# Optimization experiments

Measured on AMD Instinct MI355X. Metric: run time of the kernel, lower is better.

The kernel has to match this reference:

```python
import jax, jax.numpy as jnp
import numpy as np

N, E, R, F, HD = 4096, 2048, 4, 128, 256
DEG_EPS = 1e-8
BN_EPS = 1e-5
LN_EPS = 1e-5


def _xavier(k, shape):
    scale = np.sqrt(2.0 / (shape[-2] + shape[-1])).astype(np.float32)
    return jax.random.normal(k, shape, jnp.float32) * scale


def setup_inputs() -> dict:
    key = jax.random.key(0)
    ks = jax.random.split(key, 8)
    X = jax.random.normal(ks[0], (N, F), jnp.float32)
    # sparse binary incidence matrices, one per relation type, stacked [R,N,E]
    H = (jax.random.uniform(ks[1], (R, N, E)) < 0.05).astype(jnp.float32)
    return {
        "X": X,
        "H": H,
        "W1": _xavier(ks[2], (R, F, HD)),
        "W2": _xavier(ks[3], (R, HD, HD)),
        "W3": _xavier(ks[4], (R, HD, F)),
        "imp": jnp.ones((3, R), jnp.float32),        # relation_importance per conv layer
        "b1": jnp.zeros((HD,), jnp.float32),
        "b2": jnp.zeros((HD,), jnp.float32),
        "b3": jnp.zeros((F,), jnp.float32),
        "bn_gamma": jnp.ones((2, HD), jnp.float32),
        "bn_beta": jnp.zeros((2, HD), jnp.float32),
        "ln_gamma": jnp.ones((2, HD), jnp.float32),
        "ln_beta": jnp.zeros((2, HD), jnp.float32),
        "rel_attn": jnp.ones((R,), jnp.float32) / R,
    }


def typed_conv(X, Hw, W, imp, bias):
    # Hw: [R,N,E] weighted incidence; theta = Dv^{-1/2} H De^{-1/2} via row/col scaling
    dv = jnp.power(Hw.sum(axis=2) + DEG_EPS, -0.5)   # [R,N]
    de = jnp.power(Hw.sum(axis=1) + DEG_EPS, -0.5)   # [R,E]
    theta = Hw * dv[:, :, None] * de[:, None, :]     # [R,N,E]
    # (theta @ theta^T) @ X computed as theta @ (theta^T @ X) -- same math, no NxN
    t = jnp.einsum('rne,nf->ref', theta, X)          # [R,E,Fin]
    Hn = jnp.einsum('rne,ref->rnf', theta, t)        # [R,N,Fin]
    out = jnp.einsum('rnf,rfo->rno', Hn, W)          # [R,N,Fout]
    out = out * jax.nn.sigmoid(imp)[:, None, None]
    return out.sum(axis=0) + bias


def bn_ln_elu(X, bg, bb, lg, lb):
    # BatchNorm1d with batch statistics (biased var), then LayerNorm, then ELU
    mu = X.mean(axis=0)
    var = X.var(axis=0)
    X = (X - mu) * jax.lax.rsqrt(var + BN_EPS) * bg + bb
    m = X.mean(axis=-1, keepdims=True)
    v = X.var(axis=-1, keepdims=True)
    X = (X - m) * jax.lax.rsqrt(v + LN_EPS) * lg + lb
    return jax.nn.elu(X)


def reference(X, H, W1, W2, W3, imp, b1, b2, b3, bn_gamma, bn_beta, ln_gamma, ln_beta, rel_attn):
    rw = jax.nn.softmax(rel_attn)
    Hw = H * rw[:, None, None]                       # weighted incidence per relation
    h = typed_conv(X, Hw, W1, imp[0], b1)
    h = bn_ln_elu(h, bn_gamma[0], bn_beta[0], ln_gamma[0], ln_beta[0])
    h = typed_conv(h, Hw, W2, imp[1], b2)
    h = bn_ln_elu(h, bn_gamma[1], bn_beta[1], ln_gamma[1], ln_beta[1])
    out = typed_conv(h, Hw, W3, imp[2], b3)
    return out + X  # residual: out_channels == in_channels by construction
```

## Files before the change

### kernel.cpp

```cpp
#include <hip/hip_runtime.h>
#include <hip/hip_bf16.h>

#define NN 4096
#define EE 2048
#define RR 4
#define FF 128
#define HDD 256
#define S1 192
#define S2 320

typedef __attribute__((ext_vector_type(4))) float floatx4;
typedef __attribute__((ext_vector_type(8))) __bf16 bf16x8;
typedef __attribute__((ext_vector_type(8))) unsigned short u16x8;

#define AS1 __attribute__((address_space(1)))
#define AS3 __attribute__((address_space(3)))

__device__ __forceinline__ void async16(const void* g, void* l) {
  __builtin_amdgcn_global_load_lds((const AS1 void*)(unsigned long long)(g),
                                   (AS3 void*)(unsigned int)(unsigned long long)(l),
                                   16, 0, 0);
}

__device__ inline unsigned short f2b(float x) {
  unsigned int u = __float_as_uint(x);
  unsigned int r = u + 0x7fffu + ((u >> 16) & 1u);
  return (unsigned short)(r >> 16);
}

__device__ inline float rel_w(const float* rel, int r) {
  float m = fmaxf(fmaxf(rel[0], rel[1]), fmaxf(rel[2], rel[3]));
  float s = 0.f;
#pragma unroll
  for (int i = 0; i < RR; i++) s += expf(rel[i] - m);
  return expf(rel[r] - m) / s;
}

__global__ void k_prep1(const float* __restrict__ H, const float* __restrict__ rel,
                        const float* __restrict__ W1, const float* __restrict__ W2,
                        const float* __restrict__ W3, const float* __restrict__ imp,
                        float* __restrict__ dvs, unsigned long long* __restrict__ mask,
                        unsigned short* __restrict__ idx1, int* __restrict__ cnt1,
                        unsigned short* __restrict__ W1catT, unsigned short* __restrict__ W2T,
                        unsigned short* __restrict__ W3T, int* __restrict__ cnt2) {
  int b = blockIdx.x;
  if (b < 4096) {
    int wave = (b << 2) | (threadIdx.x >> 6);
    int lane = threadIdx.x & 63;
    int r = wave >> 12;
    const float* row = H + (size_t)wave * EE;
    unsigned long long* mrow = mask + (size_t)wave * 32;
    unsigned short* list = idx1 + (size_t)wave * S1;
    int tot = 0;
    for (int j = 0; j < 32; j++) {
      float h = row[j * 64 + lane];
      unsigned long long m = __ballot(h != 0.0f);
      if (lane == 0) mrow[j] = m;
      if (h != 0.0f) {
        int pos = tot + __popcll(m & ((1ull << lane) - 1ull));
        if (pos < S1) list[pos] = (unsigned short)(j * 64 + lane);
      }
      tot += __popcll(m);
    }
    int tc = tot < S1 ? tot : S1;
    int padded = (tc + 7) & ~7;
    if (padded == 0) padded = 8;
    unsigned short padE = (unsigned short)((RR - r) << 11);
    if (lane < padded - tc) list[tc + lane] = padE;
    if (lane == 0) {
      cnt1[wave] = tc;
      float rwr = rel_w(rel, r);
      dvs[wave] = rwr * rsqrtf(rwr * (float)tot + 1e-8f);
    }
  } else if (b < 4096 + 2048) {
    int idx = (b - 4096) * 256 + threadIdx.x;
    if (idx < RR * FF * HDD) {
      int o = idx % HDD, f = (idx / HDD) % FF, r = idx / (HDD * FF);
      float sg = 1.0f / (1.0f + expf(-imp[r]));
      W1catT[(size_t)o * (RR * FF) + r * FF + f] = f2b(sg * W1[((size_t)r * FF + f) * HDD + o]);
    } else if (idx < RR * FF * HDD + RR * HDD * HDD) {
      int j = idx - RR * FF * HDD;
      int c = j % HDD, o = (j / HDD) % HDD, r = j / (HDD * HDD);
      float sg = 1.0f / (1.0f + expf(-imp[RR + r]));
      W2T[j] = f2b(sg * W2[((size_t)r * HDD + c) * HDD + o]);
    } else {
      int j = idx - RR * FF * HDD - RR * HDD * HDD;
      int c = j % HDD, o = (j / HDD) % FF, r = j / (HDD * FF);
      float sg = 1.0f / (1.0f + expf(-imp[2 * RR + r]));
      W3T[j] = f2b(sg * W3[((size_t)r * HDD + c) * FF + o]);
    }
  } else {
    int i = (b - 6144) * 256 + threadIdx.x;
    if (i < RR * EE) cnt2[i] = 0;
  }
}

__global__ void k_prep2(const unsigned long long* __restrict__ m1, int* __restrict__ cnt2,
                        unsigned short* __restrict__ idx2, const float* __restrict__ X,
                        const float* __restrict__ dvs, unsigned short* __restrict__ Xdv) {
  __shared__ unsigned long long w[64 * 33];
  int t = threadIdx.x;
  if (blockIdx.x < 256) {
    int r = blockIdx.x >> 6;
    int n0 = (blockIdx.x & 63) << 6;
    const unsigned long long* src = m1 + ((size_t)(r << 12) + n0) * 32;
#pragma unroll
    for (int i = 0; i < 8; i++) {
      int idx = t + i * 256;
      int n = idx >> 5, W = idx & 31;
      w[n * 33 + W] = src[idx];
    }
    __syncthreads();
    int wid = t >> 6, lane = t & 63;
#pragma unroll
    for (int Wi = 0; Wi < 8; Wi++) {
      int W = wid * 8 + Wi;
      unsigned long long myw = w[lane * 33 + W];
      unsigned long long out = 0;
      for (int bb = 0; bb < 64; bb++) {
        unsigned long long mm = __ballot(((myw >> bb) & 1ull) != 0);
        if (lane == bb) out = mm;
      }
      if (out) {
        int e = W * 64 + lane;
        int rowid = (r << 11) + e;
        int c = __popcll(out);
        int off = atomicAdd(&cnt2[rowid], c);
        unsigned long long bb2 = out;
        while (bb2) {
          int l = __builtin_ctzll(bb2);
          bb2 &= bb2 - 1;
          if (off < S2) idx2[(size_t)rowid * S2 + off] = (unsigned short)(n0 + l);
          off++;
        }
      }
    }
  } else {
    int g = (blockIdx.x - 256) * 256 + t;
    int f8 = g & 15, n = (g >> 4) & (NN - 1), r = g >> 16;
    const float* xp = X + (size_t)n * FF + (f8 << 3);
    float4 v0 = *(const float4*)xp;
    float4 v1 = *(const float4*)(xp + 4);
    float d = dvs[(r << 12) + n];
    ushort4 o0, o1;
    o0.x = f2b(v0.x * d); o0.y = f2b(v0.y * d); o0.z = f2b(v0.z * d); o0.w = f2b(v0.w * d);
    o1.x = f2b(v1.x * d); o1.y = f2b(v1.y * d); o1.z = f2b(v1.z * d); o1.w = f2b(v1.w * d);
    unsigned short* dp = Xdv + ((size_t)(r << 12) + n) * FF + (f8 << 3);
    *(ushort4*)dp = o0;
    *(ushort4*)(dp + 4) = o1;
  }
}

__global__ void k_prep3(int* __restrict__ cnt2, unsigned short* __restrict__ idx2,
                        unsigned short* __restrict__ Xdv, unsigned short* __restrict__ hwdv,
                        unsigned short* __restrict__ ydv, unsigned short* __restrict__ t1,
                        unsigned short* __restrict__ t2, unsigned short* __restrict__ t3,
                        unsigned short* __restrict__ Z1) {
  int b = blockIdx.x, t = threadIdx.x;
  if (b < 32) {
    int row = (b << 8) + t;
    int r = row >> 11;
    int cnt = cnt2[row];
    if (cnt > S2) { cnt = S2; cnt2[row] = S2; }
    int padded = (cnt + 7) & ~7;
    if (padded == 0) padded = 8;
    unsigned short pv = (unsigned short)((RR - r) << 12);
    for (int i = cnt; i < padded; i++) idx2[(size_t)row * S2 + i] = pv;
  } else {
    int q = b - 32;
    unsigned short* p; int C;
    switch (q) {
      case 0: p = Xdv  + (size_t)(RR * NN) * FF;  C = FF;  break;
      case 1: p = hwdv + (size_t)(RR * NN) * HDD; C = HDD; break;
      case 2: p = ydv  + (size_t)(RR * NN) * FF;  C = FF;  break;
      case 3: p = t1   + (size_t)(RR * EE) * FF;  C = FF;  break;
      case 4: p = t2   + (size_t)(RR * EE) * HDD; C = HDD; break;
      case 5: p = t3   + (size_t)(RR * EE) * FF;  C = FF;  break;
      default: p = Z1  + (size_t)(RR * EE) * HDD; C = HDD; break;
    }
    if (t < C) p[t] = 0;
  }
}

__global__ __launch_bounds__(256) void k_gemm3(
    const unsigned short* __restrict__ A, const unsigned short* __restrict__ BT,
    int K, int lda, int ldb, long a_rs, long b_rs,
    unsigned short* __restrict__ P, long c_rs, int ldc,
    const float* __restrict__ rscale, long rs_rs) {
  __shared__ unsigned short Al[2][128 * 64];
  __shared__ unsigned short Bl[2][128 * 64];
  int tid = threadIdx.x, wid = tid >> 6, lane = tid & 63;
  int m0 = blockIdx.x << 7, n0 = blockIdx.y << 7;
  int zr = blockIdx.z;
  int r8 = lane >> 3, c8 = lane & 7;
  int swz = ((c8 ^ r8) << 3);
  const unsigned short* Ab = A + (size_t)zr * a_rs + (size_t)m0 * lda;
  const unsigned short* Bb = BT + (size_t)zr * b_rs + (size_t)n0 * ldb;
  auto stage = [&](int pb, int k0) {
#pragma unroll
    for (int t = 0; t < 4; t++) {
      int rbase = (wid << 5) + (t << 3);
      int row = rbase + r8;
      async16(Ab + (size_t)row * lda + k0 + swz, &Al[pb][rbase * 64 + lane * 8]);
      async16(Bb + (size_t)row * ldb + k0 + swz, &Bl[pb][rbase * 64 + lane * 8]);
    }
  };
  int wm = (wid >> 1) << 6, wn = (wid & 1) << 6;
  int fm = lane & 15, quad = lane >> 4;
  int f7 = fm & 7;
  floatx4 acc[4][4];
#pragma unroll
  for (int i = 0; i < 4; i++)
#pragma unroll
    for (int j = 0; j < 4; j++) acc[i][j] = (floatx4){0.f, 0.f, 0.f, 0.f};
  auto compute = [&](int pb) {
#pragma unroll
    for (int ks = 0; ks < 2; ks++) {
      int kg = (ks << 2) | quad;
      int ko = ((kg ^ f7) << 3);
      bf16x8 a[4], b[4];
#pragma unroll
      for (int i = 0; i < 4; i++) {
        a[i] = *(const bf16x8*)&Al[pb][(wm + i * 16 + fm) * 64 + ko];
        b[i] = *(const bf16x8*)&Bl[pb][(wn + i * 16 + fm) * 64 + ko];
      }
#pragma unroll
      for (int i = 0; i < 4; i++)
#pragma unroll
        for (int j = 0; j < 4; j++)
          acc[i][j] = __builtin_amdgcn_mfma_f32_16x16x32_bf16(a[i], b[j], acc[i][j], 0, 0, 0);
    }
  };
  stage(0, 0);
  __syncthreads();
  for (int k0 = 0; k0 < K; k0 += 128) {
    if (k0 + 64 < K) stage(1, k0 + 64);
    compute(0);
    __syncthreads();
    if (k0 + 128 < K) stage(0, k0 + 128);
    compute(1);
    __syncthreads();
  }
  unsigned short* Cb = P + (size_t)zr * c_rs;
#pragma unroll
  for (int mi = 0; mi < 4; mi++)
#pragma unroll
    for (int v = 0; v < 4; v++) {
      int row = m0 + wm + mi * 16 + quad * 4 + v;
      float rs = rscale ? rscale[(size_t)zr * rs_rs + row] : 1.0f;
#pragma unroll
      for (int ni = 0; ni < 4; ni++) {
        int col = n0 + wn + ni * 16 + fm;
        Cb[(size_t)row * ldc + col] = f2b(acc[mi][ni][v] * rs);
      }
    }
}

template <int C>
__global__ __launch_bounds__(256) void k_b2s(
    const int* __restrict__ cnt2, const unsigned short* __restrict__ idx2,
    const unsigned short* __restrict__ T, const float* __restrict__ rel,
    unsigned short* __restrict__ out, float* __restrict__ csz) {
  if (blockIdx.x == 0) { csz[threadIdx.x] = 0.f; csz[threadIdx.x + 256] = 0.f; }
  int wid = threadIdx.x >> 6, lane = threadIdx.x & 63;
  int wv = (blockIdx.x << 2) | wid;
  int r = wv >> 11;
  int cnt = cnt2[wv];
  const unsigned short* list = idx2 + (size_t)wv * S2;
  const unsigned short* Tb = T + ((size_t)(r << 12)) * C;
  int lo = (C == 256) ? (lane << 2) : (lane << 1);
  float a0 = 0.f, a1 = 0.f, a2 = 0.f, a3 = 0.f;
  int nb = (cnt + 7) >> 3;
  uint2 u[8];
  {
    u16x8 I = *(const u16x8*)list;
#pragma unroll
    for (int k = 0; k < 8; k++) {
      const unsigned short* p = Tb + (size_t)((unsigned short)I[k]) * C + lo;
      if (C == 256) u[k] = *(const uint2*)p;
      else { u[k].x = *(const unsigned int*)p; u[k].y = 0; }
    }
  }
  for (int b = 0; b < nb; b++) {
    int bn = (b + 1 < nb) ? b + 1 : b;
    u16x8 I = *(const u16x8*)(list + (bn << 3));
    uint2 un[8];
#pragma unroll
    for (int k = 0; k < 8; k++) {
      const unsigned short* p = Tb + (size_t)((unsigned short)I[k]) * C + lo;
      if (C == 256) un[k] = *(const uint2*)p;
      else { un[k].x = *(const unsigned int*)p; un[k].y = 0; }
    }
#pragma unroll
    for (int k = 0; k < 8; k++) {
      a0 += __uint_as_float(u[k].x << 16);
      a1 += __uint_as_float(u[k].x & 0xffff0000u);
      if (C == 256) {
        a2 += __uint_as_float(u[k].y << 16);
        a3 += __uint_as_float(u[k].y & 0xffff0000u);
      }
    }
#pragma unroll
    for (int k = 0; k < 8; k++) u[k] = un[k];
  }
  float rwr = rel_w(rel, r);
  float s = 1.0f / (rwr * (float)cnt + 1e-8f);
  unsigned short* op = out + (size_t)wv * C;
  if (C == 256) {
    ushort4 o;
    o.x = f2b(a0 * s); o.y = f2b(a1 * s); o.z = f2b(a2 * s); o.w = f2b(a3 * s);
    *(ushort4*)(op + (lane << 2)) = o;
  } else {
    ushort2 o;
    o.x = f2b(a0 * s); o.y = f2b(a1 * s);
    *(ushort2*)(op + (lane << 1)) = o;
  }
}

__global__ __launch_bounds__(256) void k_b1s256(
    const int* __restrict__ cnt1, const unsigned short* __restrict__ idx1,
    const unsigned short* __restrict__ T, const float* __restrict__ dvs,
    float* __restrict__ out) {
  __shared__ float sm[4][256];
  int wid = threadIdx.x >> 6, lane = threadIdx.x & 63;
  int n = blockIdx.x;
  int rn = (wid << 12) + n;
  int cnt = cnt1[rn];
  const unsigned short* list = idx1 + (size_t)rn * S1;
  const unsigned short* Tb = T + ((size_t)(wid << 11)) * 256;
  float a0 = 0.f, a1 = 0.f, a2 = 0.f, a3 = 0.f;
  int nb = (cnt + 7) >> 3;
  uint2 u[8];
  {
    u16x8 I = *(const u16x8*)list;
#pragma unroll
    for (int k = 0; k < 8; k++)
      u[k] = *(const uint2*)(Tb + (size_t)((unsigned short)I[k]) * 256 + (lane << 2));
  }
  for (int b = 0; b < nb; b++) {
    int bn = (b + 1 < nb) ? b + 1 : b;
    u16x8 I = *(const u16x8*)(list + (bn << 3));
    uint2 un[8];
#pragma unroll
    for (int k = 0; k < 8; k++)
      un[k] = *(const uint2*)(Tb + (size_t)((unsigned short)I[k]) * 256 + (lane << 2));
#pragma unroll
    for (int k = 0; k < 8; k++) {
      a0 += __uint_as_float(u[k].x << 16);
      a1 += __uint_as_float(u[k].x & 0xffff0000u);
      a2 += __uint_as_float(u[k].y << 16);
      a3 += __uint_as_float(u[k].y & 0xffff0000u);
    }
#pragma unroll
    for (int k = 0; k < 8; k++) u[k] = un[k];
  }
  float dv = dvs[rn];
  float4 yv = {dv * a0, dv * a1, dv * a2, dv * a3};
  *(float4*)&sm[wid][lane << 2] = yv;
  __syncthreads();
  int c = threadIdx.x;
  out[(size_t)n * HDD + c] = sm[0][c] + sm[1][c] + sm[2][c] + sm[3][c];
}

__global__ __launch_bounds__(256) void k_b1s128o(
    const int* __restrict__ cnt1, const unsigned short* __restrict__ idx1,
    const unsigned short* __restrict__ T, const float* __restrict__ dvs,
    const float* __restrict__ X, const float* __restrict__ b3, float* __restrict__ out) {
  __shared__ float sm[4][128];
  int wid = threadIdx.x >> 6, lane = threadIdx.x & 63;
  int n = blockIdx.x;
  int rn = (wid << 12) + n;
  int cnt = cnt1[rn];
  const unsigned short* list = idx1 + (size_t)rn * S1;
  const unsigned short* Tb = T + ((size_t)(wid << 11)) * 128;
  float a0 = 0.f, a1 = 0.f;
  int nb = (cnt + 7) >> 3;
  unsigned int u[8];
  {
    u16x8 I = *(const u16x8*)list;
#pragma unroll
    for (int k = 0; k < 8; k++)
      u[k] = *(const unsigned int*)(Tb + (size_t)((unsigned short)I[k]) * 128 + (lane << 1));
  }
  for (int b = 0; b < nb; b++) {
    int bn = (b + 1 < nb) ? b + 1 : b;
    u16x8 I = *(const u16x8*)(list + (bn << 3));
    unsigned int un[8];
#pragma unroll
    for (int k = 0; k < 8; k++)
      un[k] = *(const unsigned int*)(Tb + (size_t)((unsigned short)I[k]) * 128 + (lane << 1));
#pragma unroll
    for (int k = 0; k < 8; k++) {
      a0 += __uint_as_float(u[k] << 16);
      a1 += __uint_as_float(u[k] & 0xffff0000u);
    }
#pragma unroll
    for (int k = 0; k < 8; k++) u[k] = un[k];
  }
  float dv = dvs[rn];
  float2 yv = {dv * a0, dv * a1};
  *(float2*)&sm[wid][lane << 1] = yv;
  __syncthreads();
  int t = threadIdx.x;
  if (t < 128) {
    float y = sm[0][t] + sm[1][t] + sm[2][t] + sm[3][t];
    out[(size_t)n * FF + t] = X[(size_t)n * FF + t] + b3[t] + y;
  }
}

__global__ void k_stats(const float* __restrict__ x, float* __restrict__ cs) {
  __shared__ float sm[2][8][256];
  int cg = (threadIdx.x & 31) << 3;
  int rowt = threadIdx.x >> 5;
  int r0 = blockIdx.x * 32;
  float s[8] = {0, 0, 0, 0, 0, 0, 0, 0}, s2[8] = {0, 0, 0, 0, 0, 0, 0, 0};
  for (int j = 0; j < 4; j++) {
    const float* p = x + (size_t)(r0 + rowt * 4 + j) * HDD + cg;
    float4 v0 = *(const float4*)p;
    float4 v1 = *(const float4*)(p + 4);
    float vv[8] = {v0.x, v0.y, v0.z, v0.w, v1.x, v1.y, v1.z, v1.w};
#pragma unroll
    for (int i = 0; i < 8; i++) { s[i] += vv[i]; s2[i] += vv[i] * vv[i]; }
  }
#pragma unroll
  for (int i = 0; i < 8; i++) { sm[0][rowt][cg + i] = s[i]; sm[1][rowt][cg + i] = s2[i]; }
  __syncthreads();
  int c = threadIdx.x;
  float a0 = 0, a1 = 0;
#pragma unroll
  for (int t = 0; t < 8; t++) { a0 += sm[0][t][c]; a1 += sm[1][t][c]; }
  atomicAdd(&cs[c], a0);
  atomicAdd(&cs[c + 256], a1);
}

__global__ void k_bnlnelu(const float* __restrict__ x, const float* __restrict__ cs,
                          const float* __restrict__ bg, const float* __restrict__ bb,
                          const float* __restrict__ lg, const float* __restrict__ lb,
                          unsigned short* __restrict__ out) {
  int wid = threadIdx.x >> 6, lane = threadIdx.x & 63;
  int n = blockIdx.x * 4 + wid;
  float y[4];
  float m = 0.f;
#pragma unroll
  for (int j = 0; j < 4; j++) {
    int c = lane + 64 * j;
    float mu = cs[c] * (1.0f / NN);
    float var = cs[c + 256] * (1.0f / NN) - mu * mu;
    float xv = x[(size_t)n * HDD + c];
    y[j] = (xv - mu) * rsqrtf(var + 1e-5f) * bg[c] + bb[c];
    m += y[j];
  }
  for (int off = 32; off; off >>= 1) m += __shfl_down(m, off);
  m = __shfl(m, 0) * (1.0f / HDD);
  float var = 0.f;
#pragma unroll
  for (int j = 0; j < 4; j++) { float d = y[j] - m; var += d * d; }
  for (int off = 32; off; off >>= 1) var += __shfl_down(var, off);
  var = __shfl(var, 0) * (1.0f / HDD);
  float inv = rsqrtf(var + 1e-5f);
#pragma unroll
  for (int j = 0; j < 4; j++) {
    int c = lane + 64 * j;
    float z = (y[j] - m) * inv * lg[c] + lb[c];
    z = z > 0.f ? z : expm1f(z);
    out[(size_t)n * HDD + c] = f2b(z);
  }
}

extern "C" void kernel_launch(void* const* d_in, const int* in_sizes, int n_in,
                              void* d_out, int out_size, void* d_ws, size_t ws_size,
                              hipStream_t stream) {
  const float* X   = (const float*)d_in[0];
  const float* H   = (const float*)d_in[1];
  const float* W1  = (const float*)d_in[2];
  const float* W2  = (const float*)d_in[3];
  const float* W3  = (const float*)d_in[4];
  const float* imp = (const float*)d_in[5];
  const float* b3  = (const float*)d_in[8];
  const float* bng = (const float*)d_in[9];
  const float* bnb = (const float*)d_in[10];
  const float* lng = (const float*)d_in[11];
  const float* lnb = (const float*)d_in[12];
  const float* rel = (const float*)d_in[13];
  (void)in_sizes; (void)n_in; (void)out_size; (void)ws_size;

  char* w = (char*)d_ws;
  size_t off = 0;
  auto alloc = [&](size_t bytes) -> void* {
    void* p = w + off;
    off += (bytes + 255) & ~(size_t)255;
    return p;
  };
  float* dvs   = (float*)alloc((size_t)RR * NN * 4);
  float* csbuf = (float*)alloc(512 * 4);
  int* cnt1    = (int*)alloc((size_t)RR * NN * 4);
  int* cnt2    = (int*)alloc((size_t)RR * EE * 4);
  unsigned long long* mask1 = (unsigned long long*)alloc((size_t)RR * NN * 32 * 8);
  unsigned short* idx1 = (unsigned short*)alloc((size_t)RR * NN * S1 * 2);
  unsigned short* idx2 = (unsigned short*)alloc((size_t)RR * EE * S2 * 2);
  unsigned short* Xdv  = (unsigned short*)alloc(((size_t)RR * NN + 1) * FF * 2);
  unsigned short* t1   = (unsigned short*)alloc(((size_t)RR * EE + 1) * FF * 2);
  unsigned short* Z1   = (unsigned short*)alloc(((size_t)RR * EE + 1) * HDD * 2);
  float* convout       = (float*)alloc((size_t)NN * HDD * 4);
  unsigned short* Xb   = (unsigned short*)alloc((size_t)NN * HDD * 2);
  unsigned short* hwdv = (unsigned short*)alloc(((size_t)RR * NN + 1) * HDD * 2);
  unsigned short* t2   = (unsigned short*)alloc(((size_t)RR * EE + 1) * HDD * 2);
  unsigned short* ydv  = (unsigned short*)alloc(((size_t)RR * NN + 1) * FF * 2);
  unsigned short* t3   = (unsigned short*)alloc(((size_t)RR * EE + 1) * FF * 2);
  unsigned short* W1catT = (unsigned short*)alloc((size_t)RR * FF * HDD * 2);
  unsigned short* W2T    = (unsigned short*)alloc((size_t)RR * HDD * HDD * 2);
  unsigned short* W3T    = (unsigned short*)alloc((size_t)RR * HDD * FF * 2);

  k_prep1<<<4096 + 2048 + 32, 256, 0, stream>>>(H, rel, W1, W2, W3, imp,
                                                dvs, mask1, idx1, cnt1, W1catT, W2T, W3T, cnt2);
  k_prep2<<<256 + 1024, 256, 0, stream>>>(mask1, cnt2, idx2, X, dvs, Xdv);
  k_prep3<<<32 + 7, 256, 0, stream>>>(cnt2, idx2, Xdv, hwdv, ydv, t1, t2, t3, Z1);

  k_b2s<128><<<2048, 256, 0, stream>>>(cnt2, idx2, Xdv, rel, t1, csbuf);
  k_gemm3<<<dim3(EE / 128, HDD / 128, RR), 256, 0, stream>>>(
      t1, W1catT, FF, FF, RR * FF, (long)EE * FF, FF, Z1, (long)EE * HDD, HDD, nullptr, 0);
  k_b1s256<<<NN, 256, 0, stream>>>(cnt1, idx1, Z1, dvs, convout);
  k_stats<<<NN / 32, 256, 0, stream>>>(convout, csbuf);
  k_bnlnelu<<<NN / 4, 256, 0, stream>>>(convout, csbuf, bng, bnb, lng, lnb, Xb);

  k_gemm3<<<dim3(NN / 128, HDD / 128, RR), 256, 0, stream>>>(
      Xb, W2T, HDD, HDD, HDD, 0, (long)HDD * HDD, hwdv, (long)NN * HDD, HDD, dvs, NN);
  k_b2s<256><<<2048, 256, 0, stream>>>(cnt2, idx2, hwdv, rel, t2, csbuf);
  k_b1s256<<<NN, 256, 0, stream>>>(cnt1, idx1, t2, dvs, convout);
  k_stats<<<NN / 32, 256, 0, stream>>>(convout, csbuf);
  k_bnlnelu<<<NN / 4, 256, 0, stream>>>(convout, csbuf, bng + HDD, bnb + HDD, lng + HDD, lnb + HDD, Xb);

  k_gemm3<<<dim3(NN / 128, 1, RR), 256, 0, stream>>>(
      Xb, W3T, HDD, HDD, HDD, 0, (long)FF * HDD, ydv, (long)NN * FF, FF, dvs, NN);
  k_b2s<128><<<2048, 256, 0, stream>>>(cnt2, idx2, ydv, rel, t3, csbuf);
  k_b1s128o<<<NN, 256, 0, stream>>>(cnt1, idx1, t3, dvs, X, b3, (float*)d_out);
}
```

Baseline: 565.0 us.

## Double-buffer gather loops, remap b2s blocks per XCD, fuse BN stats into gather

The sparse-gather kernels now alternate between two register buffers, so the gathers for two batches ahead are in flight while the current one accumulates. Index lists are padded to at least 24 so the pipeline prologue stays in bounds. k_b2s maps blocks so that each XCD handles one relation's half of the edges, aiming for better L2 locality. The separate column-statistics kernel is removed; k_b1s256 atomically adds column sums and sums of squares into 8 striped partial buffers, which the BN kernel then adds together. This removes one pass over convout and one launch per layer, at the cost of more atomics and more register pressure.

```diff
diff --git a/kernel.cpp b/kernel.cpp
--- a/kernel.cpp
+++ b/kernel.cpp
@@ -64,7 +64,7 @@
     }
     int tc = tot < S1 ? tot : S1;
     int padded = (tc + 7) & ~7;
-    if (padded == 0) padded = 8;
+    if (padded < 24) padded = 24;
     unsigned short padE = (unsigned short)((RR - r) << 11);
     if (lane < padded - tc) list[tc + lane] = padE;
     if (lane == 0) {
@@ -163,7 +163,7 @@
     int cnt = cnt2[row];
     if (cnt > S2) { cnt = S2; cnt2[row] = S2; }
     int padded = (cnt + 7) & ~7;
-    if (padded == 0) padded = 8;
+    if (padded < 24) padded = 24;
     unsigned short pv = (unsigned short)((RR - r) << 12);
     for (int i = cnt; i < padded; i++) idx2[(size_t)row * S2 + i] = pv;
   } else {
@@ -261,47 +261,58 @@
     const int* __restrict__ cnt2, const unsigned short* __restrict__ idx2,
     const unsigned short* __restrict__ T, const float* __restrict__ rel,
     unsigned short* __restrict__ out, float* __restrict__ csz) {
-  if (blockIdx.x == 0) { csz[threadIdx.x] = 0.f; csz[threadIdx.x + 256] = 0.f; }
+  if (blockIdx.x == 0) {
+#pragma unroll
+    for (int i = 0; i < 16; i++) csz[i * 256 + threadIdx.x] = 0.f;
+  }
   int wid = threadIdx.x >> 6, lane = threadIdx.x & 63;
-  int wv = (blockIdx.x << 2) | wid;
-  int r = wv >> 11;
+  int bid = blockIdx.x;
+  int xcd = bid & 7;
+  int r = xcd >> 1;
+  int e = ((xcd & 1) << 10) + ((bid >> 3) << 2) + wid;
+  int wv = (r << 11) + e;
   int cnt = cnt2[wv];
   const unsigned short* list = idx2 + (size_t)wv * S2;
   const unsigned short* Tb = T + ((size_t)(r << 12)) * C;
   int lo = (C == 256) ? (lane << 2) : (lane << 1);
   float a0 = 0.f, a1 = 0.f, a2 = 0.f, a3 = 0.f;
   int nb = (cnt + 7) >> 3;
-  uint2 u[8];
-  {
-    u16x8 I = *(const u16x8*)list;
+  if (nb < 3) nb = 3;
+  uint2 u[8], v[8];
+  auto LIDX = [&](int bo) { return *(const u16x8*)(list + (bo << 3)); };
+  auto GATH = [&](uint2 (&d)[8], u16x8 I) {
 #pragma unroll
     for (int k = 0; k < 8; k++) {
       const unsigned short* p = Tb + (size_t)((unsigned short)I[k]) * C + lo;
-      if (C == 256) u[k] = *(const uint2*)p;
-      else { u[k].x = *(const unsigned int*)p; u[k].y = 0; }
-    }
-  }
-  for (int b = 0; b < nb; b++) {
-    int bn = (b + 1 < nb) ? b + 1 : b;
-    u16x8 I = *(const u16x8*)(list + (bn << 3));
-    uint2 un[8];
+      if (C == 256) d[k] = *(const uint2*)p;
+      else d[k].x = *(const unsigned int*)p;
+    }
+  };
+  auto ACCU = [&](uint2 (&d)[8]) {
 #pragma unroll
     for (int k = 0; k < 8; k++) {
-      const unsigned short* p = Tb + (size_t)((unsigned short)I[k]) * C + lo;
-      if (C == 256) un[k] = *(const uint2*)p;
-      else { un[k].x = *(const unsigned int*)p; un[k].y = 0; }
-    }
-#pragma unroll
-    for (int k = 0; k < 8; k++) {
-      a0 += __uint_as_float(u[k].x << 16);
-      a1 += __uint_as_float(u[k].x & 0xffff0000u);
+      a0 += __uint_as_float(d[k].x << 16);
+      a1 += __uint_as_float(d[k].x & 0xffff0000u);
       if (C == 256) {
-        a2 += __uint_as_float(u[k].y << 16);
-        a3 += __uint_as_float(u[k].y & 0xffff0000u);
+        a2 += __uint_as_float(d[k].y << 16);
+        a3 += __uint_as_float(d[k].y & 0xffff0000u);
       }
     }
-#pragma unroll
-    for (int k = 0; k < 8; k++) u[k] = un[k];
+  };
+  u16x8 iA = LIDX(0), iB = LIDX(1);
+  GATH(u, iA);
+  iA = LIDX(2);
+  GATH(v, iB);
+  iB = LIDX(3 < nb - 1 ? 3 : nb - 1);
+  for (int b = 0; b < nb; b += 2) {
+    ACCU(u);
+    if (b + 2 < nb) GATH(u, iA);
+    if (b + 4 < nb) iA = LIDX(b + 4);
+    if (b + 1 < nb) {
+      ACCU(v);
+      if (b + 3 < nb) GATH(v, iB);
+      if (b + 5 < nb) iB = LIDX(b + 5);
+    }
   }
   float rwr = rel_w(rel, r);
   float s = 1.0f / (rwr * (float)cnt + 1e-8f);
@@ -320,7 +331,7 @@
 __global__ __launch_bounds__(256) void k_b1s256(
     const int* __restrict__ cnt1, const unsigned short* __restrict__ idx1,
     const unsigned short* __restrict__ T, const float* __restrict__ dvs,
-    float* __restrict__ out) {
+    float* __restrict__ out, float* __restrict__ csbuf) {
   __shared__ float sm[4][256];
   int wid = threadIdx.x >> 6, lane = threadIdx.x & 63;
   int n = blockIdx.x;
@@ -330,36 +341,48 @@
   const unsigned short* Tb = T + ((size_t)(wid << 11)) * 256;
   float a0 = 0.f, a1 = 0.f, a2 = 0.f, a3 = 0.f;
   int nb = (cnt + 7) >> 3;
-  uint2 u[8];
-  {
-    u16x8 I = *(const u16x8*)list;
+  if (nb < 3) nb = 3;
+  uint2 u[8], v[8];
+  auto LIDX = [&](int bo) { return *(const u16x8*)(list + (bo << 3)); };
+  auto GATH = [&](uint2 (&d)[8], u16x8 I) {
 #pragma unroll
     for (int k = 0; k < 8; k++)
-      u[k] = *(const uint2*)(Tb + (size_t)((unsigned short)I[k]) * 256 + (lane << 2));
-  }
-  for (int b = 0; b < nb; b++) {
-    int bn = (b + 1 < nb) ? b + 1 : b;
-    u16x8 I = *(const u16x8*)(list + (bn << 3));
-    uint2 un[8];
-#pragma unroll
-    for (int k = 0; k < 8; k++)
-      un[k] = *(const uint2*)(Tb + (size_t)((unsigned short)I[k]) * 256 + (lane << 2));
+      d[k] = *(const uint2*)(Tb + (size_t)((unsigned short)I[k]) * 256 + (lane << 2));
+  };
+  auto ACCU = [&](uint2 (&d)[8]) {
 #pragma unroll
     for (int k = 0; k < 8; k++) {
-      a0 += __uint_as_float(u[k].x << 16);
-      a1 += __uint_as_float(u[k].x & 0xffff0000u);
-      a2 += __uint_as_float(u[k].y << 16);
-      a3 += __uint_as_float(u[k].y & 0xffff0000u);
-    }
-#pragma unroll
-    for (int k = 0; k < 8; k++) u[k] = un[k];
+      a0 += __uint_as_float(d[k].x << 16);
+      a1 += __uint_as_float(d[k].x & 0xffff0000u);
+      a2 += __uint_as_float(d[k].y << 16);
+      a3 += __uint_as_float(d[k].y & 0xffff0000u);
+    }
+  };
+  u16x8 iA = LIDX(0), iB = LIDX(1);
+  GATH(u, iA);
+  iA = LIDX(2);
+  GATH(v, iB);
+  iB = LIDX(3 < nb - 1 ? 3 : nb - 1);
+  for (int b = 0; b < nb; b += 2) {
+    ACCU(u);
+    if (b + 2 < nb) GATH(u, iA);
+    if (b + 4 < nb) iA = LIDX(b + 4);
+    if (b + 1 < nb) {
+      ACCU(v);
+      if (b + 3 < nb) GATH(v, iB);
+      if (b + 5 < nb) iB = LIDX(b + 5);
+    }
   }
   float dv = dvs[rn];
   float4 yv = {dv * a0, dv * a1, dv * a2, dv * a3};
   *(float4*)&sm[wid][lane << 2] = yv;
   __syncthreads();
   int c = threadIdx.x;
-  out[(size_t)n * HDD + c] = sm[0][c] + sm[1][c] + sm[2][c] + sm[3][c];
+  float y = sm[0][c] + sm[1][c] + sm[2][c] + sm[3][c];
+  out[(size_t)n * HDD + c] = y;
+  float* csb = csbuf + ((blockIdx.x & 7) << 9);
+  atomicAdd(&csb[c], y);
+  atomicAdd(&csb[c + 256], y * y);
 }
 
 __global__ __launch_bounds__(256) void k_b1s128o(
@@ -375,27 +398,35 @@
   const unsigned short* Tb = T + ((size_t)(wid << 11)) * 128;
   float a0 = 0.f, a1 = 0.f;
   int nb = (cnt + 7) >> 3;
-  unsigned int u[8];
-  {
-    u16x8 I = *(const u16x8*)list;
+  if (nb < 3) nb = 3;
+  unsigned int u[8], v[8];
+  auto LIDX = [&](int bo) { return *(const u16x8*)(list + (bo << 3)); };
+  auto GATH = [&](unsigned int (&d)[8], u16x8 I) {
 #pragma unroll
     for (int k = 0; k < 8; k++)
-      u[k] = *(const unsigned int*)(Tb + (size_t)((unsigned short)I[k]) * 128 + (lane << 1));
-  }
-  for (int b = 0; b < nb; b++) {
-    int bn = (b + 1 < nb) ? b + 1 : b;
-    u16x8 I = *(const u16x8*)(list + (bn << 3));
-    unsigned int un[8];
-#pragma unroll
-    for (int k = 0; k < 8; k++)
-      un[k] = *(const unsigned int*)(Tb + (size_t)((unsigned short)I[k]) * 128 + (lane << 1));
+      d[k] = *(const unsigned int*)(Tb + (size_t)((unsigned short)I[k]) * 128 + (lane << 1));
+  };
+  auto ACCU = [&](unsigned int (&d)[8]) {
 #pragma unroll
     for (int k = 0; k < 8; k++) {
-      a0 += __uint_as_float(u[k] << 16);
-      a1 += __uint_as_float(u[k] & 0xffff0000u);
-    }
-#pragma unroll
-    for (int k = 0; k < 8; k++) u[k] = un[k];
+      a0 += __uint_as_float(d[k] << 16);
+      a1 += __uint_as_float(d[k] & 0xffff0000u);
+    }
+  };
+  u16x8 iA = LIDX(0), iB = LIDX(1);
+  GATH(u, iA);
+  iA = LIDX(2);
+  GATH(v, iB);
+  iB = LIDX(3 < nb - 1 ? 3 : nb - 1);
+  for (int b = 0; b < nb; b += 2) {
+    ACCU(u);
+    if (b + 2 < nb) GATH(u, iA);
+    if (b + 4 < nb) iA = LIDX(b + 4);
+    if (b + 1 < nb) {
+      ACCU(v);
+      if (b + 3 < nb) GATH(v, iB);
+      if (b + 5 < nb) iB = LIDX(b + 5);
+    }
   }
   float dv = dvs[rn];
   float2 yv = {dv * a0, dv * a1};
@@ -408,32 +439,7 @@
   }
 }
 
-__global__ void k_stats(const float* __restrict__ x, float* __restrict__ cs) {
-  __shared__ float sm[2][8][256];
-  int cg = (threadIdx.x & 31) << 3;
-  int rowt = threadIdx.x >> 5;
-  int r0 = blockIdx.x * 32;
-  float s[8] = {0, 0, 0, 0, 0, 0, 0, 0}, s2[8] = {0, 0, 0, 0, 0, 0, 0, 0};
-  for (int j = 0; j < 4; j++) {
-    const float* p = x + (size_t)(r0 + rowt * 4 + j) * HDD + cg;
-    float4 v0 = *(const float4*)p;
-    float4 v1 = *(const float4*)(p + 4);
-    float vv[8] = {v0.x, v0.y, v0.z, v0.w, v1.x, v1.y, v1.z, v1.w};
-#pragma unroll
-    for (int i = 0; i < 8; i++) { s[i] += vv[i]; s2[i] += vv[i] * vv[i]; }
-  }
-#pragma unroll
-  for (int i = 0; i < 8; i++) { sm[0][rowt][cg + i] = s[i]; sm[1][rowt][cg + i] = s2[i]; }
-  __syncthreads();
-  int c = threadIdx.x;
-  float a0 = 0, a1 = 0;
-#pragma unroll
-  for (int t = 0; t < 8; t++) { a0 += sm[0][t][c]; a1 += sm[1][t][c]; }
-  atomicAdd(&cs[c], a0);
-  atomicAdd(&cs[c + 256], a1);
-}
-
-__global__ void k_bnlnelu(const float* __restrict__ x, const float* __restrict__ cs,
+__global__ void k_bnlnelu(const float* __restrict__ x, const float* __restrict__ csbuf,
                           const float* __restrict__ bg, const float* __restrict__ bb,
                           const float* __restrict__ lg, const float* __restrict__ lb,
                           unsigned short* __restrict__ out) {
@@ -444,8 +450,14 @@
 #pragma unroll
   for (int j = 0; j < 4; j++) {
     int c = lane + 64 * j;
-    float mu = cs[c] * (1.0f / NN);
-    float var = cs[c + 256] * (1.0f / NN) - mu * mu;
+    float s0 = 0.f, s1 = 0.f;
+#pragma unroll
+    for (int k = 0; k < 8; k++) {
+      s0 += csbuf[k * 512 + c];
+      s1 += csbuf[k * 512 + 256 + c];
+    }
+    float mu = s0 * (1.0f / NN);
+    float var = s1 * (1.0f / NN) - mu * mu;
     float xv = x[(size_t)n * HDD + c];
     y[j] = (xv - mu) * rsqrtf(var + 1e-5f) * bg[c] + bb[c];
     m += y[j];
@@ -492,7 +504,7 @@
     return p;
   };
   float* dvs   = (float*)alloc((size_t)RR * NN * 4);
-  float* csbuf = (float*)alloc(512 * 4);
+  float* csbuf = (float*)alloc(8 * 512 * 4);
   int* cnt1    = (int*)alloc((size_t)RR * NN * 4);
   int* cnt2    = (int*)alloc((size_t)RR * EE * 4);
   unsigned long long* mask1 = (unsigned long long*)alloc((size_t)RR * NN * 32 * 8);
@@ -519,15 +531,13 @@
   k_b2s<128><<<2048, 256, 0, stream>>>(cnt2, idx2, Xdv, rel, t1, csbuf);
   k_gemm3<<<dim3(EE / 128, HDD / 128, RR), 256, 0, stream>>>(
       t1, W1catT, FF, FF, RR * FF, (long)EE * FF, FF, Z1, (long)EE * HDD, HDD, nullptr, 0);
-  k_b1s256<<<NN, 256, 0, stream>>>(cnt1, idx1, Z1, dvs, convout);
-  k_stats<<<NN / 32, 256, 0, stream>>>(convout, csbuf);
+  k_b1s256<<<NN, 256, 0, stream>>>(cnt1, idx1, Z1, dvs, convout, csbuf);
   k_bnlnelu<<<NN / 4, 256, 0, stream>>>(convout, csbuf, bng, bnb, lng, lnb, Xb);
 
   k_gemm3<<<dim3(NN / 128, HDD / 128, RR), 256, 0, stream>>>(
       Xb, W2T, HDD, HDD, HDD, 0, (long)HDD * HDD, hwdv, (long)NN * HDD, HDD, dvs, NN);
   k_b2s<256><<<2048, 256, 0, stream>>>(cnt2, idx2, hwdv, rel, t2, csbuf);
-  k_b1s256<<<NN, 256, 0, stream>>>(cnt1, idx1, t2, dvs, convout);
-  k_stats<<<NN / 32, 256, 0, stream>>>(convout, csbuf);
+  k_b1s256<<<NN, 256, 0, stream>>>(cnt1, idx1, t2, dvs, convout, csbuf);
   k_bnlnelu<<<NN / 4, 256, 0, stream>>>(convout, csbuf, bng + HDD, bnb + HDD, lng + HDD, lnb + HDD, Xb);
 
   k_gemm3<<<dim3(NN / 128, 1, RR), 256, 0, stream>>>(
```

Measured after the change: 556.3 us. No clear change (-1.5%).
